# Performance work log

Hardware: AMD Instinct MI355X
Metric: run time of the kernel (lower is better)

The kernel has to match this reference:

```python
import jax, jax.numpy as jnp
import numpy as np

B, S, HID, NH, HD = 2, 8192, 768, 12, 64
BLOCK, NRAND = 64, 3


def _make_attn_indices():
    # Mirrors SparseSelfAttention.bigbird_attention index construction:
    # globals = first block + last block tokens; randoms = NRAND per block.
    rng = np.random.default_rng(0)
    glob = np.concatenate([np.arange(BLOCK), np.arange(S - BLOCK, S)])
    rand = [rng.permutation(BLOCK)[:NRAND] + i * BLOCK for i in range(S // BLOCK)]
    idx = np.unique(np.concatenate([glob] + rand))
    return jnp.asarray(idx, dtype=jnp.int32)


def setup_inputs() -> dict:
    key = jax.random.key(0)
    ks = jax.random.split(key, 6)
    w = lambda k: jax.random.normal(k, (HID, HID), jnp.float32) * 0.02
    return {
        "hidden_states": jax.random.normal(ks[0], (B, S, HID), jnp.float32),
        "attn_indices": _make_attn_indices(),
        "Wq": w(ks[1]), "bq": jnp.zeros((HID,), jnp.float32),
        "Wk": w(ks[2]), "bk": jnp.zeros((HID,), jnp.float32),
        "Wv": w(ks[3]), "bv": jnp.zeros((HID,), jnp.float32),
        "Wo": w(ks[4]), "bo": jnp.zeros((HID,), jnp.float32),
    }


def reference(hidden_states, attn_indices, Wq, bq, Wk, bk, Wv, bv, Wo, bo):
    # torch nn.Linear: y = x @ W.T + b
    heads = lambda x: x.reshape(B, S, NH, HD).transpose(0, 2, 1, 3)  # [B,H,S,d]
    q = heads(hidden_states @ Wq.T + bq)
    k = heads(hidden_states @ Wk.T + bk)
    v = heads(hidden_states @ Wv.T + bv)

    sel_q = q[:, :, attn_indices]  # gather selected queries [B,H,Nsel,d]
    scores = jnp.einsum('bhqd,bhkd->bhqk', sel_q, k) / jnp.sqrt(jnp.float32(HD))
    probs = jax.nn.softmax(scores, axis=-1)              # [B,H,Nsel,S]
    ctx = jnp.einsum('bhqk,bhkd->bhqd', probs, v)        # [B,H,Nsel,d]

    # scatter back into zeros (non-selected query positions stay zero)
    full = jnp.zeros_like(q).at[:, :, attn_indices].set(ctx)
    context = full.transpose(0, 2, 1, 3).reshape(B, S, HID)
    output = context @ Wo.T + bo
    return (output, probs)
```

## Files before the change

kernel.cpp:

```cpp
#include <hip/hip_runtime.h>
#include <hip/hip_bf16.h>

#define B_   2
#define S_   8192
#define HID_ 768
#define NH_  12
#define HD_  64

#define KC1 512
#define NC1 (S_ / KC1)
#define KC2 512
#define NC2 (S_ / KC2)

typedef __attribute__((ext_vector_type(8))) short short8;
typedef __attribute__((ext_vector_type(4))) float f32x4;

__device__ __forceinline__ ushort f2b(float x) {
    __hip_bfloat16 h = __float2bfloat16(x);
    return *reinterpret_cast<ushort*>(&h);
}

__device__ __forceinline__ int swzb(int row, int colbyte, int rowbytes) {
    return row * rowbytes + (colbyte ^ ((row & 7) << 4));
}

__device__ __forceinline__ void glds16(const ushort* g, ushort* l) {
    __builtin_amdgcn_global_load_lds(
        (__attribute__((address_space(1))) unsigned int*)g,
        (__attribute__((address_space(3))) unsigned int*)l, 16, 0, 0);
}

__global__ void fill_bias_kernel(float* __restrict__ out, const float* __restrict__ bo) {
    const int total = B_ * S_ * (HID_ / 4);
    const float4* b4 = reinterpret_cast<const float4*>(bo);
    float4* o4 = reinterpret_cast<float4*>(out);
    for (int i = blockIdx.x * blockDim.x + threadIdx.x; i < total; i += gridDim.x * blockDim.x) {
        o4[i] = b4[i % (HID_ / 4)];
    }
}

__global__ void f32_to_bf16_kernel(const float* __restrict__ in, ushort* __restrict__ out,
                                   int n4, float scale) {
    const float4* i4 = reinterpret_cast<const float4*>(in);
    ushort4* o4 = reinterpret_cast<ushort4*>(out);
    for (int i = blockIdx.x * blockDim.x + threadIdx.x; i < n4; i += gridDim.x * blockDim.x) {
        float4 v = i4[i];
        ushort4 o;
        o.x = f2b(v.x * scale);
        o.y = f2b(v.y * scale);
        o.z = f2b(v.z * scale);
        o.w = f2b(v.w * scale);
        o4[i] = o;
    }
}

__global__ void conv_weights_kernel(const float* __restrict__ Wk, const float* __restrict__ Wv,
                                    const float* __restrict__ Wq, const float* __restrict__ Wo,
                                    ushort* __restrict__ Wkb, ushort* __restrict__ Wvb,
                                    ushort* __restrict__ Wqb, ushort* __restrict__ Wob) {
    int which = blockIdx.y;
    const float* src = which == 0 ? Wk : (which == 1 ? Wv : (which == 2 ? Wq : Wo));
    ushort* dst = which == 0 ? Wkb : (which == 1 ? Wvb : (which == 2 ? Wqb : Wob));
    float scale = (which == 2) ? 0.125f : 1.0f;
    const int n4 = HID_ * HID_ / 4;
    const float4* i4 = reinterpret_cast<const float4*>(src);
    ushort4* o4 = reinterpret_cast<ushort4*>(dst);
    for (int i = blockIdx.x * blockDim.x + threadIdx.x; i < n4; i += gridDim.x * blockDim.x) {
        float4 v = i4[i];
        ushort4 o;
        o.x = f2b(v.x * scale);
        o.y = f2b(v.y * scale);
        o.z = f2b(v.z * scale);
        o.w = f2b(v.w * scale);
        o4[i] = o;
    }
}

__global__ void gather_qb_kernel(const ushort* __restrict__ Hb, const int* __restrict__ idx,
                                 ushort* __restrict__ Qinb, int nq, int nqpad) {
    int m = blockIdx.x;
    int b = m / nqpad, qi = m - b * nqpad;
    uint4* dst = reinterpret_cast<uint4*>(Qinb + (size_t)m * HID_);
    if (qi < nq) {
        int srow = b * S_ + idx[qi];
        const uint4* src = reinterpret_cast<const uint4*>(Hb + (size_t)srow * HID_);
        dst[threadIdx.x] = src[threadIdx.x];
    } else {
        dst[threadIdx.x] = make_uint4(0, 0, 0, 0);
    }
}

enum { GST_KV = 0, GST_PLAIN = 1, GST_SCATF32 = 2 };

template<int MODE>
__launch_bounds__(256)
__global__ void gemm_bf16_kernel(const ushort* __restrict__ A, const ushort* __restrict__ W,
                                 const float* __restrict__ bias, float bscale,
                                 ushort* __restrict__ C, float* __restrict__ Cf,
                                 const int* __restrict__ idx, int nq, int Mq) {
    __shared__ __align__(16) ushort As[128 * 64];
    __shared__ __align__(16) ushort Ws[128 * 64];
    const int t = threadIdx.x;
    const int lane = t & 63, w = t >> 6;
    const int wr = w >> 1, wc = w & 1;
    const int m0 = blockIdx.x * 128;
    const int n0 = blockIdx.y * 128;

    f32x4 acc[4][4];
    #pragma unroll
    for (int i = 0; i < 4; ++i)
        #pragma unroll
        for (int j = 0; j < 4; ++j) acc[i][j] = (f32x4){0.f, 0.f, 0.f, 0.f};

    for (int k0 = 0; k0 < HID_; k0 += 64) {
        __syncthreads();
        #pragma unroll
        for (int it = 0; it < 4; ++it) {
            int sid = t + it * 256;
            int row = sid >> 3, seg = sid & 7;
            int cb = (seg * 16) ^ ((row & 7) << 4);
            glds16(A + (size_t)(m0 + row) * HID_ + k0 + cb / 2, (ushort*)((char*)As + sid * 16));
            glds16(W + (size_t)(n0 + row) * HID_ + k0 + cb / 2, (ushort*)((char*)Ws + sid * 16));
        }
        __syncthreads();

        short8 af[4][2], bf_[4][2];
        #pragma unroll
        for (int mi = 0; mi < 4; ++mi)
            #pragma unroll
            for (int kh = 0; kh < 2; ++kh)
                af[mi][kh] = *reinterpret_cast<const short8*>(
                    (char*)As + swzb(wr * 64 + mi * 16 + (lane & 15), (lane >> 4) * 16 + kh * 64, 128));
        #pragma unroll
        for (int ni = 0; ni < 4; ++ni)
            #pragma unroll
            for (int kh = 0; kh < 2; ++kh)
                bf_[ni][kh] = *reinterpret_cast<const short8*>(
                    (char*)Ws + swzb(wc * 64 + ni * 16 + (lane & 15), (lane >> 4) * 16 + kh * 64, 128));

        #pragma unroll
        for (int mi = 0; mi < 4; ++mi)
            #pragma unroll
            for (int ni = 0; ni < 4; ++ni) {
                acc[mi][ni] = __builtin_amdgcn_mfma_f32_16x16x32_bf16(af[mi][0], bf_[ni][0], acc[mi][ni], 0, 0, 0);
                acc[mi][ni] = __builtin_amdgcn_mfma_f32_16x16x32_bf16(af[mi][1], bf_[ni][1], acc[mi][ni], 0, 0, 0);
            }
    }

    float bl[4];
    #pragma unroll
    for (int ni = 0; ni < 4; ++ni)
        bl[ni] = bias[n0 + wc * 64 + ni * 16 + (lane & 15)] * bscale;

    #pragma unroll
    for (int mi = 0; mi < 4; ++mi) {
        #pragma unroll
        for (int ni = 0; ni < 4; ++ni) {
            int n = n0 + wc * 64 + ni * 16 + (lane & 15);
            #pragma unroll
            for (int r = 0; r < 4; ++r) {
                int m = m0 + wr * 64 + mi * 16 + (lane >> 4) * 4 + r;
                float fv = acc[mi][ni][r] + bl[ni];
                if (MODE == GST_KV) {
                    int b = m >> 13, s = m & (S_ - 1);
                    int h = n >> 6, d = n & 63;
                    C[(((size_t)(b * NH_ + h)) * S_ + s) * HD_ + d] = f2b(fv);
                } else if (MODE == GST_PLAIN) {
                    C[(size_t)m * HID_ + n] = f2b(fv);
                } else {
                    if (m < Mq) {
                        int b = m / nq, qi = m - b * nq;
                        int srow = b * S_ + idx[qi];
                        Cf[(size_t)srow * HID_ + n] = fv;
                    }
                }
            }
        }
    }
}

__global__ void transpose_v_kernel(const ushort* __restrict__ V, ushort* __restrict__ Vt) {
    __shared__ ushort tile[64][72];
    int bh = blockIdx.y;
    int k0 = blockIdx.x * 64;
    int t = threadIdx.x;
    const ushort* src = V + (size_t)bh * S_ * HD_ + (size_t)k0 * HD_;
    #pragma unroll
    for (int it = 0; it < 2; ++it) {
        int sid = t + it * 256;
        int key = sid >> 3, seg = sid & 7;
        *reinterpret_cast<uint4*>(&tile[key][seg * 8]) =
            *reinterpret_cast<const uint4*>(src + (size_t)key * HD_ + seg * 8);
    }
    __syncthreads();
    ushort* dst = Vt + (size_t)bh * HD_ * S_ + k0;
    #pragma unroll
    for (int it = 0; it < 2; ++it) {
        int sid = t + it * 256;
        int d = sid >> 3, seg = sid & 7;
        ushort tmp[8];
        #pragma unroll
        for (int j = 0; j < 8; ++j) tmp[j] = tile[seg * 8 + j][d];
        *reinterpret_cast<uint4*>(dst + (size_t)d * S_ + seg * 8) = *reinterpret_cast<uint4*>(tmp);
    }
}

__launch_bounds__(512)
__global__ void attn_pass1_mfma(const ushort* __restrict__ Qsel, const ushort* __restrict__ Kb,
                                float2* __restrict__ mlp, int nq, int nqpad) {
    __shared__ __align__(16) ushort Ks[128 * 64];
    const int t = threadIdx.x;
    const int lane = t & 63, w = t >> 6;
    const int chunk = blockIdx.x, bh = blockIdx.y;
    const int b = bh / NH_, h = bh - b * NH_;
    const int nqt = nqpad >> 7;

    short8 qa[4][2];
    #pragma unroll
    for (int qt = 0; qt < 4; ++qt) {
        if (qt < nqt) {
            const ushort* qp = Qsel + (size_t)(b * nqpad + qt * 128 + 16 * w + (lane & 15)) * HID_
                               + h * HD_ + (lane >> 4) * 8;
            qa[qt][0] = *reinterpret_cast<const short8*>(qp);
            qa[qt][1] = *reinterpret_cast<const short8*>(qp + 32);
        }
    }

    float m_r[4][4], l_r[4][4];
    #pragma unroll
    for (int qt = 0; qt < 4; ++qt)
        #pragma unroll
        for (int r = 0; r < 4; ++r) { m_r[qt][r] = -1e30f; l_r[qt][r] = 0.f; }

    const ushort* kbase = Kb + (size_t)bh * S_ * HD_;

    for (int kb = 0; kb < KC1; kb += 128) {
        int k0 = chunk * KC1 + kb;
        __syncthreads();
        #pragma unroll
        for (int it = 0; it < 2; ++it) {
            int sid = t + it * 512;
            int row = sid >> 3, seg = sid & 7;
            int cb = (seg * 16) ^ ((row & 7) << 4);
            glds16(kbase + (size_t)(k0 + row) * HD_ + cb / 2, (ushort*)((char*)Ks + sid * 16));
        }
        __syncthreads();

        short8 kf[8][2];
        #pragma unroll
        for (int ns = 0; ns < 8; ++ns) {
            kf[ns][0] = *reinterpret_cast<const short8*>((char*)Ks + swzb(ns * 16 + (lane & 15), (lane >> 4) * 16, 128));
            kf[ns][1] = *reinterpret_cast<const short8*>((char*)Ks + swzb(ns * 16 + (lane & 15), (lane >> 4) * 16 + 64, 128));
        }

        #pragma unroll
        for (int qt = 0; qt < 4; ++qt) {
            if (qt >= nqt) continue;
            f32x4 sf[8];
            __builtin_amdgcn_s_setprio(1);
            #pragma unroll
            for (int ns = 0; ns < 8; ++ns) {
                f32x4 acc = {0.f, 0.f, 0.f, 0.f};
                acc = __builtin_amdgcn_mfma_f32_16x16x32_bf16(qa[qt][0], kf[ns][0], acc, 0, 0, 0);
                acc = __builtin_amdgcn_mfma_f32_16x16x32_bf16(qa[qt][1], kf[ns][1], acc, 0, 0, 0);
                sf[ns] = acc;
            }
            __builtin_amdgcn_s_setprio(0);
            #pragma unroll
            for (int r = 0; r < 4; ++r) {
                float bm = sf[0][r];
                #pragma unroll
                for (int ns = 1; ns < 8; ++ns) bm = fmaxf(bm, sf[ns][r]);
                float mn = fmaxf(m_r[qt][r], bm);
                float sum = 0.f;
                #pragma unroll
                for (int ns = 0; ns < 8; ++ns) sum += __expf(sf[ns][r] - mn);
                l_r[qt][r] = l_r[qt][r] * __expf(m_r[qt][r] - mn) + sum;
                m_r[qt][r] = mn;
            }
        }
    }

    #pragma unroll
    for (int qt = 0; qt < 4; ++qt) {
        if (qt >= nqt) continue;
        #pragma unroll
        for (int r = 0; r < 4; ++r) {
            float m = m_r[qt][r], l = l_r[qt][r];
            #pragma unroll
            for (int off = 1; off < 16; off <<= 1) {
                float om = __shfl_xor(m, off);
                float ol = __shfl_xor(l, off);
                float mn = fmaxf(m, om);
                l = l * __expf(m - mn) + ol * __expf(om - mn);
                m = mn;
            }
            if ((lane & 15) == 0) {
                int row = qt * 128 + 16 * w + 4 * (lane >> 4) + r;
                mlp[(size_t)chunk * (B_ * NH_ * nqpad) + (size_t)bh * nqpad + row] = make_float2(m, l);
            }
        }
    }
}

__global__ void ml_reduce_kernel(const float2* __restrict__ mlp, float2* __restrict__ ml, int nqpad) {
    int i = blockIdx.x * blockDim.x + threadIdx.x;
    int total = B_ * NH_ * nqpad;
    if (i >= total) return;
    float m = -1e30f, l = 0.f;
    #pragma unroll
    for (int c = 0; c < NC1; ++c) {
        float2 v = mlp[(size_t)c * total + i];
        float mn = fmaxf(m, v.x);
        l = l * __expf(m - mn) + v.y * __expf(v.x - mn);
        m = mn;
    }
    ml[i] = make_float2(m, l);
}

__launch_bounds__(512)
__global__ void attn_pass2_mfma(const ushort* __restrict__ Qsel, const ushort* __restrict__ Kb,
                                const ushort* __restrict__ Vtb, const float2* __restrict__ ml,
                                float* __restrict__ probs, float* __restrict__ ctxp, int nq, int nqpad) {
    __shared__ __align__(16) ushort Ks[128 * 64];
    __shared__ __align__(16) ushort Vs[64 * 128];
    __shared__ __align__(16) ushort Ps[128 * 128];
    __shared__ float mls[512], ils[512];
    const int t = threadIdx.x;
    const int lane = t & 63, w = t >> 6;
    const int chunk = blockIdx.x, bh = blockIdx.y;
    const int b = bh / NH_, h = bh - b * NH_;
    const int nqt = nqpad >> 7;

    short8 qa[4][2];
    #pragma unroll
    for (int qt = 0; qt < 4; ++qt) {
        if (qt < nqt) {
            const ushort* qp = Qsel + (size_t)(b * nqpad + qt * 128 + 16 * w + (lane & 15)) * HID_
                               + h * HD_ + (lane >> 4) * 8;
            qa[qt][0] = *reinterpret_cast<const short8*>(qp);
            qa[qt][1] = *reinterpret_cast<const short8*>(qp + 32);
        }
    }

    if (t < nqpad) {
        float2 v = ml[(size_t)bh * nqpad + t];
        mls[t] = v.x;
        ils[t] = 1.f / v.y;
    }

    const ushort* kbase  = Kb  + (size_t)bh * S_ * HD_;
    const ushort* vtbase = Vtb + (size_t)bh * HD_ * S_;
    const size_t prow0 = (size_t)bh * nq;

    f32x4 accc[4][4];
    #pragma unroll
    for (int qt = 0; qt < 4; ++qt)
        #pragma unroll
        for (int d = 0; d < 4; ++d) accc[qt][d] = (f32x4){0.f, 0.f, 0.f, 0.f};

    for (int kb = 0; kb < KC2; kb += 128) {
        int k0 = chunk * KC2 + kb;
        __syncthreads();
        #pragma unroll
        for (int it = 0; it < 2; ++it) {
            int sid = t + it * 512;
            int row = sid >> 3, seg = sid & 7;
            int cb = (seg * 16) ^ ((row & 7) << 4);
            glds16(kbase + (size_t)(k0 + row) * HD_ + cb / 2, (ushort*)((char*)Ks + sid * 16));
        }
        #pragma unroll
        for (int it = 0; it < 2; ++it) {
            int sid = t + it * 512;
            int row = sid >> 4, seg = sid & 15;
            int cb = (seg * 16) ^ ((row & 7) << 4);
            glds16(vtbase + (size_t)row * S_ + k0 + cb / 2, (ushort*)((char*)Vs + sid * 16));
        }
        __syncthreads();

        #pragma unroll
        for (int qt = 0; qt < 4; ++qt) {
            if (qt >= nqt) continue;
            float mrq[4], ilq[4];
            #pragma unroll
            for (int r = 0; r < 4; ++r) {
                int row = qt * 128 + 16 * w + 4 * (lane >> 4) + r;
                mrq[r] = mls[row];
                ilq[r] = ils[row];
            }
            __builtin_amdgcn_s_setprio(1);
            #pragma unroll
            for (int ns = 0; ns < 8; ++ns) {
                short8 b0 = *reinterpret_cast<const short8*>((char*)Ks + swzb(ns * 16 + (lane & 15), (lane >> 4) * 16, 128));
                short8 b1 = *reinterpret_cast<const short8*>((char*)Ks + swzb(ns * 16 + (lane & 15), (lane >> 4) * 16 + 64, 128));
                f32x4 acc = {0.f, 0.f, 0.f, 0.f};
                acc = __builtin_amdgcn_mfma_f32_16x16x32_bf16(qa[qt][0], b0, acc, 0, 0, 0);
                acc = __builtin_amdgcn_mfma_f32_16x16x32_bf16(qa[qt][1], b1, acc, 0, 0, 0);
                #pragma unroll
                for (int r = 0; r < 4; ++r) {
                    int rl = 16 * w + 4 * (lane >> 4) + r;
                    float p = __expf(acc[r] - mrq[r]) * ilq[r];
                    int qrow = qt * 128 + rl;
                    if (qrow < nq)
                        probs[(prow0 + qrow) * (size_t)S_ + k0 + ns * 16 + (lane & 15)] = p;
                    *reinterpret_cast<ushort*>((char*)Ps + swzb(rl, (ns * 16 + (lane & 15)) * 2, 256)) = f2b(p);
                }
            }
            short8 pa[4];
            #pragma unroll
            for (int ks = 0; ks < 4; ++ks)
                pa[ks] = *reinterpret_cast<const short8*>((char*)Ps + swzb(16 * w + (lane & 15), ks * 64 + (lane >> 4) * 16, 256));
            #pragma unroll
            for (int ds = 0; ds < 4; ++ds) {
                #pragma unroll
                for (int ks = 0; ks < 4; ++ks) {
                    short8 vb = *reinterpret_cast<const short8*>((char*)Vs + swzb(ds * 16 + (lane & 15), ks * 64 + (lane >> 4) * 16, 256));
                    accc[qt][ds] = __builtin_amdgcn_mfma_f32_16x16x32_bf16(pa[ks], vb, accc[qt][ds], 0, 0, 0);
                }
            }
            __builtin_amdgcn_s_setprio(0);
        }
    }

    float* dst = ctxp + (size_t)chunk * ((size_t)B_ * nq * HID_);
    #pragma unroll
    for (int qt = 0; qt < 4; ++qt) {
        if (qt >= nqt) continue;
        #pragma unroll
        for (int ds = 0; ds < 4; ++ds) {
            #pragma unroll
            for (int r = 0; r < 4; ++r) {
                int qrow = qt * 128 + 16 * w + 4 * (lane >> 4) + r;
                if (qrow < nq)
                    dst[(size_t)(b * nq + qrow) * HID_ + h * HD_ + ds * 16 + (lane & 15)] = accc[qt][ds][r];
            }
        }
    }
}

__global__ void ctx_reduce_kernel(const float* __restrict__ ctxp, ushort* __restrict__ ctxb, int Mq) {
    const int n4 = Mq * (HID_ / 4);
    const float4* src = reinterpret_cast<const float4*>(ctxp);
    ushort4* dst = reinterpret_cast<ushort4*>(ctxb);
    for (int i = blockIdx.x * blockDim.x + threadIdx.x; i < n4; i += gridDim.x * blockDim.x) {
        float4 s = make_float4(0.f, 0.f, 0.f, 0.f);
        #pragma unroll
        for (int c = 0; c < NC2; ++c) {
            float4 v = src[(size_t)c * n4 + i];
            s.x += v.x; s.y += v.y; s.z += v.z; s.w += v.w;
        }
        ushort4 o;
        o.x = f2b(s.x); o.y = f2b(s.y); o.z = f2b(s.z); o.w = f2b(s.w);
        dst[i] = o;
    }
}

extern "C" void kernel_launch(void* const* d_in, const int* in_sizes, int n_in,
                              void* d_out, int out_size, void* d_ws, size_t ws_size,
                              hipStream_t stream) {
    const float* hidden = (const float*)d_in[0];
    const int*   idx    = (const int*)d_in[1];
    const float* Wq = (const float*)d_in[2];
    const float* bq = (const float*)d_in[3];
    const float* Wk = (const float*)d_in[4];
    const float* bk = (const float*)d_in[5];
    const float* Wv = (const float*)d_in[6];
    const float* bv = (const float*)d_in[7];
    const float* Wo = (const float*)d_in[8];
    const float* bo = (const float*)d_in[9];
    const int nq = in_sizes[1];
    const int qt128 = (nq + 127) / 128;
    const int nqpad = qt128 * 128;
    const int Mq = B_ * nq;
    const int Mqp = B_ * nqpad;

    float* out   = (float*)d_out;
    float* probs = out + (size_t)B_ * S_ * HID_;

    char* ws = (char*)d_ws;
    const size_t kvN = (size_t)B_ * NH_ * S_ * HD_;
    ushort* Hb    = (ushort*)ws;                 ws += kvN * 2;
    ushort* K_buf = (ushort*)ws;                 ws += kvN * 2;
    ushort* V_buf = (ushort*)ws;                 ws += kvN * 2;
    ushort* Vt    = (ushort*)ws;                 ws += kvN * 2;
    ushort* Wkb   = (ushort*)ws;                 ws += (size_t)HID_ * HID_ * 2;
    ushort* Wvb   = (ushort*)ws;                 ws += (size_t)HID_ * HID_ * 2;
    ushort* Wqb   = (ushort*)ws;                 ws += (size_t)HID_ * HID_ * 2;
    ushort* Wob   = (ushort*)ws;                 ws += (size_t)HID_ * HID_ * 2;
    ushort* Qinb  = (ushort*)ws;                 ws += (size_t)Mqp * HID_ * 2;
    ushort* Qsel  = (ushort*)ws;                 ws += (size_t)Mqp * HID_ * 2;
    ushort* ctxb  = (ushort*)ws;                 ws += (size_t)Mqp * HID_ * 2;
    float*  ctxp  = (float*)ws;                  ws += (size_t)NC2 * Mq * HID_ * 4;
    float2* mlp   = (float2*)ws;                 ws += (size_t)NC1 * B_ * NH_ * nqpad * 8;
    float2* ml    = (float2*)ws;                 ws += (size_t)B_ * NH_ * nqpad * 8;

    fill_bias_kernel<<<2048, 256, 0, stream>>>(out, bo);

    f32_to_bf16_kernel<<<2048, 256, 0, stream>>>(hidden, Hb, (int)(kvN / 4), 1.0f);
    conv_weights_kernel<<<dim3(192, 4), 256, 0, stream>>>(Wk, Wv, Wq, Wo, Wkb, Wvb, Wqb, Wob);

    gather_qb_kernel<<<Mqp, 96, 0, stream>>>(Hb, idx, Qinb, nq, nqpad);

    dim3 gKV(B_ * S_ / 128, HID_ / 128);
    gemm_bf16_kernel<GST_KV><<<gKV, 256, 0, stream>>>(Hb, Wkb, bk, 1.0f, K_buf, nullptr, nullptr, 0, 0);
    gemm_bf16_kernel<GST_KV><<<gKV, 256, 0, stream>>>(Hb, Wvb, bv, 1.0f, V_buf, nullptr, nullptr, 0, 0);

    transpose_v_kernel<<<dim3(S_ / 64, B_ * NH_), 256, 0, stream>>>(V_buf, Vt);

    dim3 gQ(Mqp / 128, HID_ / 128);
    gemm_bf16_kernel<GST_PLAIN><<<gQ, 256, 0, stream>>>(Qinb, Wqb, bq, 0.125f, Qsel, nullptr, nullptr, 0, 0);

    dim3 gA1(NC1, B_ * NH_);
    attn_pass1_mfma<<<gA1, 512, 0, stream>>>(Qsel, K_buf, mlp, nq, nqpad);

    int totalml = B_ * NH_ * nqpad;
    ml_reduce_kernel<<<(totalml + 255) / 256, 256, 0, stream>>>(mlp, ml, nqpad);

    dim3 gA2(NC2, B_ * NH_);
    attn_pass2_mfma<<<gA2, 512, 0, stream>>>(Qsel, K_buf, Vt, ml, probs, ctxp, nq, nqpad);

    ctx_reduce_kernel<<<1024, 256, 0, stream>>>(ctxp, ctxb, Mq);

    dim3 gO(Mqp / 128, HID_ / 128);
    gemm_bf16_kernel<GST_SCATF32><<<gO, 256, 0, stream>>>(ctxb, Wob, bo, 1.0f, nullptr, out, idx, nq, Mq);
}
```

Baseline: 329.4 us.

## Fuse prep kernels, merge K/V GEMM with transposed V store, split attention grid

Three conversion and bias-fill kernels become one prep kernel. The Q gather now converts directly from the fp32 hidden states. The K and V projections run in a single GEMM launch that writes V already transposed, which drops the separate transpose kernel and its intermediate buffer. Pass 1 uses smaller key chunks, and pass 2 splits each chunk's query tiles across two blocks with an XCD-aware block index mapping, so more blocks run in parallel at the cost of reloading K and V tiles twice. The transposed V store writes 4 elements per lane with a large stride, which may coalesce poorly.

```diff
diff --git a/kernel.cpp b/kernel.cpp
--- a/kernel.cpp
+++ b/kernel.cpp
@@ -7,7 +7,7 @@
 #define NH_  12
 #define HD_  64
 
-#define KC1 512
+#define KC1 256
 #define NC1 (S_ / KC1)
 #define KC2 512
 #define NC2 (S_ / KC2)
@@ -30,67 +30,144 @@
         (__attribute__((address_space(3))) unsigned int*)l, 16, 0, 0);
 }
 
-__global__ void fill_bias_kernel(float* __restrict__ out, const float* __restrict__ bo) {
-    const int total = B_ * S_ * (HID_ / 4);
-    const float4* b4 = reinterpret_cast<const float4*>(bo);
-    float4* o4 = reinterpret_cast<float4*>(out);
+#define N4H (B_ * S_ * HID_ / 4)
+#define N4W (HID_ * HID_ / 4)
+__global__ void prep_kernel(const float* __restrict__ hidden, const float* __restrict__ bo,
+                            const float* __restrict__ Wk, const float* __restrict__ Wv,
+                            const float* __restrict__ Wq, const float* __restrict__ Wo,
+                            ushort* __restrict__ Hb, float* __restrict__ out,
+                            ushort* __restrict__ Wkb, ushort* __restrict__ Wvb,
+                            ushort* __restrict__ Wqb, ushort* __restrict__ Wob) {
+    const int total = 2 * N4H + 4 * N4W;
     for (int i = blockIdx.x * blockDim.x + threadIdx.x; i < total; i += gridDim.x * blockDim.x) {
-        o4[i] = b4[i % (HID_ / 4)];
-    }
-}
-
-__global__ void f32_to_bf16_kernel(const float* __restrict__ in, ushort* __restrict__ out,
-                                   int n4, float scale) {
-    const float4* i4 = reinterpret_cast<const float4*>(in);
-    ushort4* o4 = reinterpret_cast<ushort4*>(out);
-    for (int i = blockIdx.x * blockDim.x + threadIdx.x; i < n4; i += gridDim.x * blockDim.x) {
-        float4 v = i4[i];
-        ushort4 o;
-        o.x = f2b(v.x * scale);
-        o.y = f2b(v.y * scale);
-        o.z = f2b(v.z * scale);
-        o.w = f2b(v.w * scale);
-        o4[i] = o;
-    }
-}
-
-__global__ void conv_weights_kernel(const float* __restrict__ Wk, const float* __restrict__ Wv,
-                                    const float* __restrict__ Wq, const float* __restrict__ Wo,
-                                    ushort* __restrict__ Wkb, ushort* __restrict__ Wvb,
-                                    ushort* __restrict__ Wqb, ushort* __restrict__ Wob) {
-    int which = blockIdx.y;
-    const float* src = which == 0 ? Wk : (which == 1 ? Wv : (which == 2 ? Wq : Wo));
-    ushort* dst = which == 0 ? Wkb : (which == 1 ? Wvb : (which == 2 ? Wqb : Wob));
-    float scale = (which == 2) ? 0.125f : 1.0f;
-    const int n4 = HID_ * HID_ / 4;
-    const float4* i4 = reinterpret_cast<const float4*>(src);
-    ushort4* o4 = reinterpret_cast<ushort4*>(dst);
-    for (int i = blockIdx.x * blockDim.x + threadIdx.x; i < n4; i += gridDim.x * blockDim.x) {
-        float4 v = i4[i];
-        ushort4 o;
-        o.x = f2b(v.x * scale);
-        o.y = f2b(v.y * scale);
-        o.z = f2b(v.z * scale);
-        o.w = f2b(v.w * scale);
-        o4[i] = o;
-    }
-}
-
-__global__ void gather_qb_kernel(const ushort* __restrict__ Hb, const int* __restrict__ idx,
+        if (i < N4H) {
+            float4 v = reinterpret_cast<const float4*>(hidden)[i];
+            ushort4 o = {f2b(v.x), f2b(v.y), f2b(v.z), f2b(v.w)};
+            reinterpret_cast<ushort4*>(Hb)[i] = o;
+        } else if (i < 2 * N4H) {
+            int j = i - N4H;
+            reinterpret_cast<float4*>(out)[j] = reinterpret_cast<const float4*>(bo)[j % (HID_ / 4)];
+        } else {
+            int local = i - 2 * N4H;
+            int which = local / N4W, j = local - which * N4W;
+            const float* src = which == 0 ? Wk : (which == 1 ? Wv : (which == 2 ? Wq : Wo));
+            ushort* dst = which == 0 ? Wkb : (which == 1 ? Wvb : (which == 2 ? Wqb : Wob));
+            float sc = (which == 2) ? 0.125f : 1.0f;
+            float4 v = reinterpret_cast<const float4*>(src)[j];
+            ushort4 o = {f2b(v.x * sc), f2b(v.y * sc), f2b(v.z * sc), f2b(v.w * sc)};
+            reinterpret_cast<ushort4*>(dst)[j] = o;
+        }
+    }
+}
+
+__global__ void gather_qb_kernel(const float* __restrict__ hidden, const int* __restrict__ idx,
                                  ushort* __restrict__ Qinb, int nq, int nqpad) {
     int m = blockIdx.x;
     int b = m / nqpad, qi = m - b * nqpad;
-    uint4* dst = reinterpret_cast<uint4*>(Qinb + (size_t)m * HID_);
+    int t = threadIdx.x;
+    ushort4* dst = reinterpret_cast<ushort4*>(Qinb + (size_t)m * HID_);
     if (qi < nq) {
         int srow = b * S_ + idx[qi];
-        const uint4* src = reinterpret_cast<const uint4*>(Hb + (size_t)srow * HID_);
-        dst[threadIdx.x] = src[threadIdx.x];
+        const float4* src = reinterpret_cast<const float4*>(hidden + (size_t)srow * HID_);
+        float4 a = src[t * 2], c = src[t * 2 + 1];
+        ushort4 o0 = {f2b(a.x), f2b(a.y), f2b(a.z), f2b(a.w)};
+        ushort4 o1 = {f2b(c.x), f2b(c.y), f2b(c.z), f2b(c.w)};
+        dst[t * 2] = o0;
+        dst[t * 2 + 1] = o1;
     } else {
-        dst[threadIdx.x] = make_uint4(0, 0, 0, 0);
-    }
-}
-
-enum { GST_KV = 0, GST_PLAIN = 1, GST_SCATF32 = 2 };
+        ushort4 z = {0, 0, 0, 0};
+        dst[t * 2] = z;
+        dst[t * 2 + 1] = z;
+    }
+}
+
+__launch_bounds__(256)
+__global__ void gemm_kv_kernel(const ushort* __restrict__ A,
+                               const ushort* __restrict__ Wkb, const ushort* __restrict__ Wvb,
+                               const float* __restrict__ bk, const float* __restrict__ bv,
+                               ushort* __restrict__ Kb, ushort* __restrict__ Vt) {
+    __shared__ __align__(16) ushort As[128 * 64];
+    __shared__ __align__(16) ushort Ws[128 * 64];
+    const int t = threadIdx.x;
+    const int lane = t & 63, w = t >> 6;
+    const int wr = w >> 1, wc = w & 1;
+    const int m0 = blockIdx.x * 128;
+    const bool isV = blockIdx.y >= 6;
+    const int n0 = (isV ? (blockIdx.y - 6) : blockIdx.y) * 128;
+    const ushort* W = isV ? Wvb : Wkb;
+    const float* bias = isV ? bv : bk;
+
+    f32x4 acc[4][4];
+    #pragma unroll
+    for (int i = 0; i < 4; ++i)
+        #pragma unroll
+        for (int j = 0; j < 4; ++j) acc[i][j] = (f32x4){0.f, 0.f, 0.f, 0.f};
+
+    for (int k0 = 0; k0 < HID_; k0 += 64) {
+        __syncthreads();
+        #pragma unroll
+        for (int it = 0; it < 4; ++it) {
+            int sid = t + it * 256;
+            int row = sid >> 3, seg = sid & 7;
+            int cb = (seg * 16) ^ ((row & 7) << 4);
+            glds16(A + (size_t)(m0 + row) * HID_ + k0 + cb / 2, (ushort*)((char*)As + sid * 16));
+            glds16(W + (size_t)(n0 + row) * HID_ + k0 + cb / 2, (ushort*)((char*)Ws + sid * 16));
+        }
+        __syncthreads();
+
+        short8 af[4][2], bf_[4][2];
+        #pragma unroll
+        for (int mi = 0; mi < 4; ++mi)
+            #pragma unroll
+            for (int kh = 0; kh < 2; ++kh)
+                af[mi][kh] = *reinterpret_cast<const short8*>(
+                    (char*)As + swzb(wr * 64 + mi * 16 + (lane & 15), (lane >> 4) * 16 + kh * 64, 128));
+        #pragma unroll
+        for (int ni = 0; ni < 4; ++ni)
+            #pragma unroll
+            for (int kh = 0; kh < 2; ++kh)
+                bf_[ni][kh] = *reinterpret_cast<const short8*>(
+                    (char*)Ws + swzb(wc * 64 + ni * 16 + (lane & 15), (lane >> 4) * 16 + kh * 64, 128));
+
+        #pragma unroll
+        for (int mi = 0; mi < 4; ++mi)
+            #pragma unroll
+            for (int ni = 0; ni < 4; ++ni) {
+                acc[mi][ni] = __builtin_amdgcn_mfma_f32_16x16x32_bf16(af[mi][0], bf_[ni][0], acc[mi][ni], 0, 0, 0);
+                acc[mi][ni] = __builtin_amdgcn_mfma_f32_16x16x32_bf16(af[mi][1], bf_[ni][1], acc[mi][ni], 0, 0, 0);
+            }
+    }
+
+    float bl[4];
+    #pragma unroll
+    for (int ni = 0; ni < 4; ++ni)
+        bl[ni] = bias[n0 + wc * 64 + ni * 16 + (lane & 15)];
+
+    #pragma unroll
+    for (int mi = 0; mi < 4; ++mi) {
+        #pragma unroll
+        for (int ni = 0; ni < 4; ++ni) {
+            int n = n0 + wc * 64 + ni * 16 + (lane & 15);
+            int h = n >> 6, d = n & 63;
+            int s0 = m0 + wr * 64 + mi * 16 + (lane >> 4) * 4;
+            if (isV) {
+                int b = s0 >> 13, s = s0 & (S_ - 1);
+                ushort4 o = {f2b(acc[mi][ni][0] + bl[ni]), f2b(acc[mi][ni][1] + bl[ni]),
+                             f2b(acc[mi][ni][2] + bl[ni]), f2b(acc[mi][ni][3] + bl[ni])};
+                *reinterpret_cast<ushort4*>(&Vt[((size_t)(b * NH_ + h) * HD_ + d) * S_ + s]) = o;
+            } else {
+                #pragma unroll
+                for (int r = 0; r < 4; ++r) {
+                    int m = s0 + r;
+                    int b = m >> 13, s = m & (S_ - 1);
+                    Kb[(((size_t)(b * NH_ + h)) * S_ + s) * HD_ + d] = f2b(acc[mi][ni][r] + bl[ni]);
+                }
+            }
+        }
+    }
+}
+
+enum { GST_PLAIN = 1, GST_SCATF32 = 2 };
 
 template<int MODE>
 __launch_bounds__(256)
@@ -161,11 +238,7 @@
             for (int r = 0; r < 4; ++r) {
                 int m = m0 + wr * 64 + mi * 16 + (lane >> 4) * 4 + r;
                 float fv = acc[mi][ni][r] + bl[ni];
-                if (MODE == GST_KV) {
-                    int b = m >> 13, s = m & (S_ - 1);
-                    int h = n >> 6, d = n & 63;
-                    C[(((size_t)(b * NH_ + h)) * S_ + s) * HD_ + d] = f2b(fv);
-                } else if (MODE == GST_PLAIN) {
+                if (MODE == GST_PLAIN) {
                     C[(size_t)m * HID_ + n] = f2b(fv);
                 } else {
                     if (m < Mq) {
@@ -179,39 +252,14 @@
     }
 }
 
-__global__ void transpose_v_kernel(const ushort* __restrict__ V, ushort* __restrict__ Vt) {
-    __shared__ ushort tile[64][72];
-    int bh = blockIdx.y;
-    int k0 = blockIdx.x * 64;
-    int t = threadIdx.x;
-    const ushort* src = V + (size_t)bh * S_ * HD_ + (size_t)k0 * HD_;
-    #pragma unroll
-    for (int it = 0; it < 2; ++it) {
-        int sid = t + it * 256;
-        int key = sid >> 3, seg = sid & 7;
-        *reinterpret_cast<uint4*>(&tile[key][seg * 8]) =
-            *reinterpret_cast<const uint4*>(src + (size_t)key * HD_ + seg * 8);
-    }
-    __syncthreads();
-    ushort* dst = Vt + (size_t)bh * HD_ * S_ + k0;
-    #pragma unroll
-    for (int it = 0; it < 2; ++it) {
-        int sid = t + it * 256;
-        int d = sid >> 3, seg = sid & 7;
-        ushort tmp[8];
-        #pragma unroll
-        for (int j = 0; j < 8; ++j) tmp[j] = tile[seg * 8 + j][d];
-        *reinterpret_cast<uint4*>(dst + (size_t)d * S_ + seg * 8) = *reinterpret_cast<uint4*>(tmp);
-    }
-}
-
 __launch_bounds__(512)
 __global__ void attn_pass1_mfma(const ushort* __restrict__ Qsel, const ushort* __restrict__ Kb,
                                 float2* __restrict__ mlp, int nq, int nqpad) {
     __shared__ __align__(16) ushort Ks[128 * 64];
     const int t = threadIdx.x;
     const int lane = t & 63, w = t >> 6;
-    const int chunk = blockIdx.x, bh = blockIdx.y;
+    const int lin = blockIdx.x;
+    const int chunk = lin & (NC1 - 1), bh = lin >> 5;
     const int b = bh / NH_, h = bh - b * NH_;
     const int nqt = nqpad >> 7;
 
@@ -325,39 +373,47 @@
     __shared__ __align__(16) ushort Ks[128 * 64];
     __shared__ __align__(16) ushort Vs[64 * 128];
     __shared__ __align__(16) ushort Ps[128 * 128];
-    __shared__ float mls[512], ils[512];
+    __shared__ float mls[256], ils[256];
     const int t = threadIdx.x;
     const int lane = t & 63, w = t >> 6;
-    const int chunk = blockIdx.x, bh = blockIdx.y;
+    const int lin = blockIdx.x;
+    const int xcd = lin & 7, slot = lin >> 3;
+    const int qhalf = slot & 1, pl = slot >> 1;
+    const int pair = xcd * 48 + pl;
+    const int chunk = pair & (NC2 - 1), bh = pair >> 4;
     const int b = bh / NH_, h = bh - b * NH_;
     const int nqt = nqpad >> 7;
 
-    short8 qa[4][2];
-    #pragma unroll
-    for (int qt = 0; qt < 4; ++qt) {
+    short8 qa[2][2];
+    #pragma unroll
+    for (int ql = 0; ql < 2; ++ql) {
+        int qt = qhalf * 2 + ql;
         if (qt < nqt) {
             const ushort* qp = Qsel + (size_t)(b * nqpad + qt * 128 + 16 * w + (lane & 15)) * HID_
                                + h * HD_ + (lane >> 4) * 8;
-            qa[qt][0] = *reinterpret_cast<const short8*>(qp);
-            qa[qt][1] = *reinterpret_cast<const short8*>(qp + 32);
-        }
-    }
-
-    if (t < nqpad) {
-        float2 v = ml[(size_t)bh * nqpad + t];
-        mls[t] = v.x;
-        ils[t] = 1.f / v.y;
+            qa[ql][0] = *reinterpret_cast<const short8*>(qp);
+            qa[ql][1] = *reinterpret_cast<const short8*>(qp + 32);
+        }
+    }
+
+    if (t < 256) {
+        int row = qhalf * 256 + t;
+        if (row < nqpad) {
+            float2 v = ml[(size_t)bh * nqpad + row];
+            mls[t] = v.x;
+            ils[t] = 1.f / v.y;
+        }
     }
 
     const ushort* kbase  = Kb  + (size_t)bh * S_ * HD_;
     const ushort* vtbase = Vtb + (size_t)bh * HD_ * S_;
     const size_t prow0 = (size_t)bh * nq;
 
-    f32x4 accc[4][4];
-    #pragma unroll
-    for (int qt = 0; qt < 4; ++qt)
-        #pragma unroll
-        for (int d = 0; d < 4; ++d) accc[qt][d] = (f32x4){0.f, 0.f, 0.f, 0.f};
+    f32x4 accc[2][4];
+    #pragma unroll
+    for (int ql = 0; ql < 2; ++ql)
+        #pragma unroll
+        for (int d = 0; d < 4; ++d) accc[ql][d] = (f32x4){0.f, 0.f, 0.f, 0.f};
 
     for (int kb = 0; kb < KC2; kb += 128) {
         int k0 = chunk * KC2 + kb;
@@ -379,14 +435,15 @@
         __syncthreads();
 
         #pragma unroll
-        for (int qt = 0; qt < 4; ++qt) {
+        for (int ql = 0; ql < 2; ++ql) {
+            int qt = qhalf * 2 + ql;
             if (qt >= nqt) continue;
             float mrq[4], ilq[4];
             #pragma unroll
             for (int r = 0; r < 4; ++r) {
-                int row = qt * 128 + 16 * w + 4 * (lane >> 4) + r;
-                mrq[r] = mls[row];
-                ilq[r] = ils[row];
+                int lrow = ql * 128 + 16 * w + 4 * (lane >> 4) + r;
+                mrq[r] = mls[lrow];
+                ilq[r] = ils[lrow];
             }
             __builtin_amdgcn_s_setprio(1);
             #pragma unroll
@@ -394,8 +451,8 @@
                 short8 b0 = *reinterpret_cast<const short8*>((char*)Ks + swzb(ns * 16 + (lane & 15), (lane >> 4) * 16, 128));
                 short8 b1 = *reinterpret_cast<const short8*>((char*)Ks + swzb(ns * 16 + (lane & 15), (lane >> 4) * 16 + 64, 128));
                 f32x4 acc = {0.f, 0.f, 0.f, 0.f};
-                acc = __builtin_amdgcn_mfma_f32_16x16x32_bf16(qa[qt][0], b0, acc, 0, 0, 0);
-                acc = __builtin_amdgcn_mfma_f32_16x16x32_bf16(qa[qt][1], b1, acc, 0, 0, 0);
+                acc = __builtin_amdgcn_mfma_f32_16x16x32_bf16(qa[ql][0], b0, acc, 0, 0, 0);
+                acc = __builtin_amdgcn_mfma_f32_16x16x32_bf16(qa[ql][1], b1, acc, 0, 0, 0);
                 #pragma unroll
                 for (int r = 0; r < 4; ++r) {
                     int rl = 16 * w + 4 * (lane >> 4) + r;
@@ -415,7 +472,7 @@
                 #pragma unroll
                 for (int ks = 0; ks < 4; ++ks) {
                     short8 vb = *reinterpret_cast<const short8*>((char*)Vs + swzb(ds * 16 + (lane & 15), ks * 64 + (lane >> 4) * 16, 256));
-                    accc[qt][ds] = __builtin_amdgcn_mfma_f32_16x16x32_bf16(pa[ks], vb, accc[qt][ds], 0, 0, 0);
+                    accc[ql][ds] = __builtin_amdgcn_mfma_f32_16x16x32_bf16(pa[ks], vb, accc[ql][ds], 0, 0, 0);
                 }
             }
             __builtin_amdgcn_s_setprio(0);
@@ -424,7 +481,8 @@
 
     float* dst = ctxp + (size_t)chunk * ((size_t)B_ * nq * HID_);
     #pragma unroll
-    for (int qt = 0; qt < 4; ++qt) {
+    for (int ql = 0; ql < 2; ++ql) {
+        int qt = qhalf * 2 + ql;
         if (qt >= nqt) continue;
         #pragma unroll
         for (int ds = 0; ds < 4; ++ds) {
@@ -432,7 +490,7 @@
             for (int r = 0; r < 4; ++r) {
                 int qrow = qt * 128 + 16 * w + 4 * (lane >> 4) + r;
                 if (qrow < nq)
-                    dst[(size_t)(b * nq + qrow) * HID_ + h * HD_ + ds * 16 + (lane & 15)] = accc[qt][ds][r];
+                    dst[(size_t)(b * nq + qrow) * HID_ + h * HD_ + ds * 16 + (lane & 15)] = accc[ql][ds][r];
             }
         }
     }
@@ -481,7 +539,6 @@
     const size_t kvN = (size_t)B_ * NH_ * S_ * HD_;
     ushort* Hb    = (ushort*)ws;                 ws += kvN * 2;
     ushort* K_buf = (ushort*)ws;                 ws += kvN * 2;
-    ushort* V_buf = (ushort*)ws;                 ws += kvN * 2;
     ushort* Vt    = (ushort*)ws;                 ws += kvN * 2;
     ushort* Wkb   = (ushort*)ws;                 ws += (size_t)HID_ * HID_ * 2;
     ushort* Wvb   = (ushort*)ws;                 ws += (size_t)HID_ * HID_ * 2;
@@ -494,33 +551,24 @@
     float2* mlp   = (float2*)ws;                 ws += (size_t)NC1 * B_ * NH_ * nqpad * 8;
     float2* ml    = (float2*)ws;                 ws += (size_t)B_ * NH_ * nqpad * 8;
 
-    fill_bias_kernel<<<2048, 256, 0, stream>>>(out, bo);
-
-    f32_to_bf16_kernel<<<2048, 256, 0, stream>>>(hidden, Hb, (int)(kvN / 4), 1.0f);
-    conv_weights_kernel<<<dim3(192, 4), 256, 0, stream>>>(Wk, Wv, Wq, Wo, Wkb, Wvb, Wqb, Wob);
-
-    gather_qb_kernel<<<Mqp, 96, 0, stream>>>(Hb, idx, Qinb, nq, nqpad);
-
-    dim3 gKV(B_ * S_ / 128, HID_ / 128);
-    gemm_bf16_kernel<GST_KV><<<gKV, 256, 0, stream>>>(Hb, Wkb, bk, 1.0f, K_buf, nullptr, nullptr, 0, 0);
-    gemm_bf16_kernel<GST_KV><<<gKV, 256, 0, stream>>>(Hb, Wvb, bv, 1.0f, V_buf, nullptr, nullptr, 0, 0);
-
-    transpose_v_kernel<<<dim3(S_ / 64, B_ * NH_), 256, 0, stream>>>(V_buf, Vt);
+    prep_kernel<<<2048, 256, 0, stream>>>(hidden, bo, Wk, Wv, Wq, Wo,
+                                          Hb, out, Wkb, Wvb, Wqb, Wob);
+    gather_qb_kernel<<<Mqp, 96, 0, stream>>>(hidden, idx, Qinb, nq, nqpad);
+
+    dim3 gKV(B_ * S_ / 128, 12);
+    gemm_kv_kernel<<<gKV, 256, 0, stream>>>(Hb, Wkb, Wvb, bk, bv, K_buf, Vt);
 
     dim3 gQ(Mqp / 128, HID_ / 128);
     gemm_bf16_kernel<GST_PLAIN><<<gQ, 256, 0, stream>>>(Qinb, Wqb, bq, 0.125f, Qsel, nullptr, nullptr, 0, 0);
 
-    dim3 gA1(NC1, B_ * NH_);
-    attn_pass1_mfma<<<gA1, 512, 0, stream>>>(Qsel, K_buf, mlp, nq, nqpad);
+    attn_pass1_mfma<<<NC1 * B_ * NH_, 512, 0, stream>>>(Qsel, K_buf, mlp, nq, nqpad);
 
     int totalml = B_ * NH_ * nqpad;
     ml_reduce_kernel<<<(totalml + 255) / 256, 256, 0, stream>>>(mlp, ml, nqpad);
 
-    dim3 gA2(NC2, B_ * NH_);
-    attn_pass2_mfma<<<gA2, 512, 0, stream>>>(Qsel, K_buf, Vt, ml, probs, ctxp, nq, nqpad);
+    attn_pass2_mfma<<<2 * NC2 * B_ * NH_, 512, 0, stream>>>(Qsel, K_buf, Vt, ml, probs, ctxp, nq, nqpad);
 
     ctx_reduce_kernel<<<1024, 256, 0, stream>>>(ctxp, ctxb, Mq);
 
-    dim3 gO(Mqp / 128, HID_ / 128);
-    gemm_bf16_kernel<GST_SCATF32><<<gO, 256, 0, stream>>>(ctxb, Wob, bo, 1.0f, nullptr, out, idx, nq, Mq);
-}
+    gemm_bf16_kernel<GST_SCATF32><<<gQ, 256, 0, stream>>>(ctxb, Wob, bo, 1.0f, nullptr, out, idx, nq, Mq);
+}
```

New measurement: 299.9 us. -9.0%, faster.
